# Kernel optimization log

Hardware: AMD Instinct MI355X
Metric: run time of the kernel (lower is better)

The kernel has to match this reference:

```python
import jax, jax.numpy as jnp
import numpy as np

N = 50000
E = 1_600_000
SIGMA = 0.5


def _spmm(rows, cols, vals, dense):
    # sparse [N,N] @ dense [N,D] via gather + segment_sum
    return jax.ops.segment_sum(vals[:, None] * dense[cols], rows, num_segments=N)


def _gnn_layer(h, rows, cols, vals, W, active=True):
    support = h @ W            # [N, out]
    out = _spmm(rows, cols, vals, support)
    return jax.nn.relu(out) if active else out


def setup_inputs() -> dict:
    key = jax.random.key(0)
    ks = jax.random.split(key, 14)
    dims = [512, 500, 500, 2000, 10, 10]  # n_input, enc1, enc2, enc3, n_z, n_clusters
    inp = {
        "x": jax.random.normal(ks[0], (N, dims[0]), dtype=jnp.float32),
        "adj_rows": jax.random.randint(ks[1], (E,), 0, N, dtype=jnp.int32),
        "adj_cols": jax.random.randint(ks[2], (E,), 0, N, dtype=jnp.int32),
        "adj_vals": jax.random.uniform(ks[3], (E,), dtype=jnp.float32),
        "tra1": jax.random.normal(ks[4], (N, dims[1]), dtype=jnp.float32),
        "tra2": jax.random.normal(ks[5], (N, dims[2]), dtype=jnp.float32),
        "tra3": jax.random.normal(ks[6], (N, dims[3]), dtype=jnp.float32),
        "z": jax.random.normal(ks[7], (N, dims[4]), dtype=jnp.float32),
    }
    for i in range(5):
        fan_in, fan_out = dims[i], dims[i + 1]
        bound = float(np.sqrt(6.0 / (fan_in + fan_out)))  # xavier uniform
        inp[f"W{i+1}"] = jax.random.uniform(
            ks[8 + i], (fan_in, fan_out), dtype=jnp.float32, minval=-bound, maxval=bound)
    return inp


def reference(x, adj_rows, adj_cols, adj_vals, tra1, tra2, tra3, z,
              W1, W2, W3, W4, W5):
    s = SIGMA
    h = _gnn_layer(x, adj_rows, adj_cols, adj_vals, W1)
    h = _gnn_layer((1 - s) * h + s * tra1, adj_rows, adj_cols, adj_vals, W2)
    h = _gnn_layer((1 - s) * h + s * tra2, adj_rows, adj_cols, adj_vals, W3)
    h = _gnn_layer((1 - s) * h + s * tra3, adj_rows, adj_cols, adj_vals, W4)
    h = _gnn_layer((1 - s) * h + s * z, adj_rows, adj_cols, adj_vals, W5, active=False)
    return h
```

## Files before the change

kernel.cpp:

```cpp
#include <hip/hip_runtime.h>
#include <hip/hip_bf16.h>


#define SCAN_CHUNK 512
#define BM 128
#define BN 128
#define BK 64

typedef __attribute__((ext_vector_type(4))) float f32x4;
typedef __attribute__((ext_vector_type(8))) __bf16 bf16x8;
typedef __attribute__((ext_vector_type(8))) short s16x8;

__device__ __forceinline__ bf16x8 as_bf(s16x8 v) { union { s16x8 s; bf16x8 b; } u; u.s = v; return u.b; }
__device__ __forceinline__ ushort f2bf(float f) {
    uint u = __float_as_uint(f);
    return (ushort)((u + 0x7FFFu + ((u >> 16) & 1u)) >> 16);
}
__device__ __forceinline__ float bf2f(ushort s) { return __uint_as_float(((uint)s) << 16); }

#define GLL16(g, l)                                                                 \
    __builtin_amdgcn_global_load_lds((const __attribute__((address_space(1))) void*)(g), \
                                     (__attribute__((address_space(3))) void*)(l), 16, 0, 0)

#define STAGE_TILE8(k0, base)                                                       \
    _Pragma("unroll")                                                               \
    for (int i = 0; i < 2; ++i) {                                                   \
        int ar = row0 + arow_off + i * 64;                                          \
        if (ar >= M) ar = M - 1;                                                    \
        GLL16(A + (size_t)ar * 512 + (k0) + acol, &lds[(base) + (w * 8 + i * 64) * BK]); \
        GLL16(Bt + (size_t)(col0 + arow_off + i * 64) * 512 + (k0) + acol,          \
              &lds[(base) + 8192 + (w * 8 + i * 64) * BK]);                         \
    }

#define COMPUTE_TILE8(base)                                                         \
    _Pragma("unroll")                                                               \
    for (int s = 0; s < 2; ++s) {                                                   \
        int cswz = (((s * 4 + (l >> 4)) ^ (l & 7)) << 3);                           \
        bf16x8 af[4], bfr[2];                                                       \
        _Pragma("unroll")                                                           \
        for (int m = 0; m < 4; ++m)                                                 \
            af[m] = as_bf(*(const s16x8*)&lds[(base) + (wr + m * 16 + (l & 15)) * BK + cswz]); \
        _Pragma("unroll")                                                           \
        for (int n = 0; n < 2; ++n)                                                 \
            bfr[n] = as_bf(*(const s16x8*)&lds[(base) + 8192 + (wc + n * 16 + (l & 15)) * BK + cswz]); \
        _Pragma("unroll")                                                           \
        for (int m = 0; m < 4; ++m)                                                 \
            _Pragma("unroll")                                                       \
            for (int n = 0; n < 2; ++n)                                             \
                acc[m][n] = __builtin_amdgcn_mfma_f32_16x16x32_bf16(af[m], bfr[n], acc[m][n], 0, 0, 0); \
    }

#define KLOOP_PIPELINED()                                                           \
    STAGE_TILE8(0, 0);                                                              \
    int base = 0;                                                                   \
    _Pragma("unroll 1")                                                             \
    for (int t = 0; t < 8; ++t) {                                                   \
        if (t < 7) {                                                                \
            STAGE_TILE8((t + 1) * BK, base ^ 16384);                                \
            asm volatile("s_waitcnt vmcnt(4)" ::: "memory");                        \
        } else {                                                                    \
            asm volatile("s_waitcnt vmcnt(0)" ::: "memory");                        \
        }                                                                           \
        __builtin_amdgcn_s_barrier();                                               \
        __builtin_amdgcn_sched_barrier(0);                                          \
        COMPUTE_TILE8(base);                                                        \
        __builtin_amdgcn_sched_barrier(0);                                          \
        __builtin_amdgcn_s_barrier();                                               \
        base ^= 16384;                                                              \
    }

__global__ __launch_bounds__(512) void gemm_sup(const ushort* __restrict__ A,
                                                const ushort* __restrict__ Bt,
                                                ushort* __restrict__ C, int M) {
    __shared__ ushort lds[32768];
    int tid = threadIdx.x;
    int w = tid >> 6, l = tid & 63;
    int row0 = blockIdx.y * BM, col0 = blockIdx.x * BN;
    int wr = (w >> 2) * 64, wc = (w & 3) * 32;
    f32x4 acc[4][2] = {};
    int arow_off = w * 8 + (l >> 3);
    int acol = (((l & 7) ^ (l >> 3)) << 3);

    KLOOP_PIPELINED();

    int crow = (l >> 4) * 4, ccol = l & 15;
#pragma unroll
    for (int m = 0; m < 4; ++m)
#pragma unroll
        for (int n = 0; n < 2; ++n) {
            int gc = col0 + wc + n * 16 + ccol;
#pragma unroll
            for (int r = 0; r < 4; ++r) {
                int gr = row0 + wr + m * 16 + crow + r;
                if (gr < M) C[(size_t)gr * 512 + gc] = f2bf(acc[m][n][r]);
            }
        }
}

__global__ __launch_bounds__(512) void gemm3_w4(const ushort* __restrict__ A,
                                                const ushort* __restrict__ Bt,
                                                const float* __restrict__ T,
                                                const float* __restrict__ W4,
                                                float* __restrict__ sup4p, int M) {
    __shared__ ushort lds[32768];
    int tid = threadIdx.x;
    int w = tid >> 6, l = tid & 63;
    int row0 = blockIdx.y * BM, col0 = blockIdx.x * BN;
    int wr = (w >> 2) * 64, wc = (w & 3) * 32;
    int crow = (l >> 4) * 4, ccol = l & 15;

    bf16x8 w4f;
    {
        s16x8 tmp;
#pragma unroll
        for (int kk = 0; kk < 8; ++kk) {
            int gk = col0 + (w & 3) * 32 + ((l >> 4) << 3) + kk;
            float v = (ccol < 10 && gk < 2000) ? 0.5f * W4[(size_t)gk * 10 + ccol] : 0.f;
            tmp[kk] = (short)f2bf(v);
        }
        w4f = as_bf(tmp);
    }

    f32x4 acc[4][2] = {};
    int arow_off = w * 8 + (l >> 3);
    int acol = (((l & 7) ^ (l >> 3)) << 3);

    KLOOP_PIPELINED();

    ushort* actS = lds;

    __syncthreads();
#pragma unroll
    for (int m = 0; m < 4; ++m)
#pragma unroll
        for (int n = 0; n < 2; ++n) {
            int cl = wc + n * 16 + ccol;
            int cch = cl >> 3, clo = cl & 7;
#pragma unroll
            for (int r = 0; r < 4; ++r) {
                int rl = wr + m * 16 + crow + r;
                actS[rl * 128 + (((cch ^ (rl & 7)) << 3) | clo)] = f2bf(fmaxf(acc[m][n][r], 0.f));
            }
        }
    __syncthreads();

    f32x4 acc2[4] = {};
    {
        int chunk = (w & 3) * 4 + (l >> 4);
#pragma unroll
        for (int m = 0; m < 4; ++m) {
            int row = wr + m * 16 + ccol;
            bf16x8 af = as_bf(*(const s16x8*)&actS[row * 128 + ((chunk ^ (row & 7)) << 3)]);
            acc2[m] = __builtin_amdgcn_mfma_f32_16x16x32_bf16(af, w4f, acc2[m], 0, 0, 0);
        }
    }
    __syncthreads();

    {
        int r_off = tid >> 5;
        int c4 = (tid & 31) * 4;
        int chunk = (tid & 31) >> 1;
        int lo = (tid & 1) * 4;
#pragma unroll
        for (int p = 0; p < 8; ++p) {
            int rl = p * 16 + r_off;
            int gr = row0 + rl;
            int gcb = col0 + c4;
            ushort4 h;
            if (gr < M && gcb + 3 < 2000) {
                float4 tv = *(const float4*)(T + (size_t)gr * 2000 + gcb);
                h.x = f2bf(tv.x); h.y = f2bf(tv.y); h.z = f2bf(tv.z); h.w = f2bf(tv.w);
            } else {
                float e[4];
#pragma unroll
                for (int i = 0; i < 4; ++i)
                    e[i] = (gr < M && gcb + i < 2000) ? T[(size_t)gr * 2000 + gcb + i] : 0.f;
                h.x = f2bf(e[0]); h.y = f2bf(e[1]); h.z = f2bf(e[2]); h.w = f2bf(e[3]);
            }
            *(ushort4*)&actS[rl * 128 + ((chunk ^ (rl & 7)) << 3) + lo] = h;
        }
    }
    __syncthreads();

    {
        int chunk = (w & 3) * 4 + (l >> 4);
#pragma unroll
        for (int m = 0; m < 4; ++m) {
            int row = wr + m * 16 + ccol;
            bf16x8 af = as_bf(*(const s16x8*)&actS[row * 128 + ((chunk ^ (row & 7)) << 3)]);
            acc2[m] = __builtin_amdgcn_mfma_f32_16x16x32_bf16(af, w4f, acc2[m], 0, 0, 0);
        }
    }
    __syncthreads();

    float* redS = (float*)lds;
    {
        int q = w & 3;
#pragma unroll
        for (int m = 0; m < 4; ++m)
#pragma unroll
            for (int r = 0; r < 4; ++r) {
                int row = wr + m * 16 + crow + r;
                redS[(q * 128 + row) * 16 + ccol] = acc2[m][r];
            }
    }
    __syncthreads();
    {
        float* dst = sup4p + (size_t)blockIdx.x * ((size_t)M * 10);
#pragma unroll
        for (int p = 0; p < 4; ++p) {
            int o = p * 512 + tid;
            int row = o >> 4, col = o & 15;
            int gr = row0 + row;
            if (col < 10 && gr < M) {
                float s = redS[(0 * 128 + row) * 16 + col] + redS[(1 * 128 + row) * 16 + col]
                        + redS[(2 * 128 + row) * 16 + col] + redS[(3 * 128 + row) * 16 + col];
                dst[(size_t)gr * 10 + col] = s;
            }
        }
    }
}

__global__ __launch_bounds__(256) void sup4_reduce(const float* __restrict__ P,
                                                   float* __restrict__ O, int n) {
    int i = blockIdx.x * 256 + threadIdx.x;
    if (i >= n) return;
    float s = 0.f;
#pragma unroll
    for (int j = 0; j < 16; ++j) s += P[(size_t)j * n + i];
    O[i] = s;
}

__global__ __launch_bounds__(256) void cvt4(const float* __restrict__ s,
                                            ushort* __restrict__ d, long n4) {
    long i = (long)blockIdx.x * 256 + threadIdx.x;
    if (i >= n4) return;
    float4 v = ((const float4*)s)[i];
    ushort4 o = { f2bf(v.x), f2bf(v.y), f2bf(v.z), f2bf(v.w) };
    ((ushort4*)d)[i] = o;
}

__global__ __launch_bounds__(256) void cvt_wt(const float* __restrict__ W,
                                              ushort* __restrict__ Wt,
                                              int Ksrc, int Nsrc, int Npad) {
    int i = blockIdx.x * 256 + threadIdx.x;
    if (i >= Npad * 512) return;
    int n = i >> 9, k = i & 511;
    float v = (k < Ksrc && n < Nsrc) ? W[(size_t)k * Nsrc + n] : 0.f;
    Wt[i] = f2bf(v);
}

__global__ __launch_bounds__(256) void csr_count(const int* __restrict__ rows,
                                                 int* __restrict__ cnt, int E) {
    int e = blockIdx.x * 256 + threadIdx.x;
    if (e < E) atomicAdd(&cnt[rows[e]], 1);
}

__global__ __launch_bounds__(256) void scan1(const int* __restrict__ cnt,
                                             int* __restrict__ csum, int n) {
    __shared__ int red[256];
    int base = blockIdx.x * SCAN_CHUNK;
    int t = threadIdx.x;
    int s = 0;
    if (base + t < n) s += cnt[base + t];
    if (base + t + 256 < n) s += cnt[base + t + 256];
    red[t] = s;
    __syncthreads();
    for (int off = 128; off; off >>= 1) {
        if (t < off) red[t] += red[t + off];
        __syncthreads();
    }
    if (t == 0) csum[blockIdx.x] = red[0];
}

__global__ void scan2(int* csum, int nch) {
    if (threadIdx.x == 0 && blockIdx.x == 0) {
        int acc = 0;
        for (int i = 0; i < nch; ++i) { int v = csum[i]; csum[i] = acc; acc += v; }
    }
}

__global__ __launch_bounds__(256) void scan3(const int* __restrict__ cnt,
                                             const int* __restrict__ csum,
                                             int* __restrict__ rowptr, int n, int E) {
    __shared__ int sm[SCAN_CHUNK];
    int base = blockIdx.x * SCAN_CHUNK;
    int t = threadIdx.x;
    for (int i = t; i < SCAN_CHUNK; i += 256) sm[i] = (base + i < n) ? cnt[base + i] : 0;
    __syncthreads();
    for (int off = 1; off < SCAN_CHUNK; off <<= 1) {
        int i0 = t, i1 = t + 256;
        int v0 = (i0 >= off) ? sm[i0 - off] : 0;
        int v1 = (i1 >= off) ? sm[i1 - off] : 0;
        __syncthreads();
        sm[i0] += v0;
        sm[i1] += v1;
        __syncthreads();
    }
    int off0 = csum[blockIdx.x];
    for (int i = t; i < SCAN_CHUNK; i += 256)
        if (base + i < n) rowptr[base + i] = off0 + (i ? sm[i - 1] : 0);
    if (blockIdx.x == 0 && t == 0) rowptr[n] = E;
}

__global__ __launch_bounds__(256) void csr_fill(const int* __restrict__ rows,
                                                const int* __restrict__ cols,
                                                const float* __restrict__ vals,
                                                int* __restrict__ cur,
                                                int2* __restrict__ edges, int E) {
    int e = blockIdx.x * 256 + threadIdx.x;
    if (e >= E) return;
    int p = atomicAdd(&cur[rows[e]], 1);
    edges[p] = make_int2(cols[e], __float_as_int(vals[e]));
}

__global__ __launch_bounds__(256) void spmm_bf(const int* __restrict__ rowptr,
                                               const int2* __restrict__ edges,
                                               const ushort* __restrict__ S,
                                               const float* __restrict__ T,
                                               ushort* __restrict__ O,
                                               int nrows, int domix) {
    int wid = (int)((blockIdx.x * 256 + threadIdx.x) >> 6);
    int lane = threadIdx.x & 63;
    if (wid >= nrows) return;
    int beg = rowptr[wid], end = rowptr[wid + 1];
    float acc[8] = {0.f, 0.f, 0.f, 0.f, 0.f, 0.f, 0.f, 0.f};
    int e = beg;
    for (; e + 3 < end; e += 4) {
        int2 e0 = edges[e], e1 = edges[e + 1], e2 = edges[e + 2], e3 = edges[e + 3];
        float v0 = __int_as_float(e0.y), v1 = __int_as_float(e1.y);
        float v2 = __int_as_float(e2.y), v3 = __int_as_float(e3.y);
        s16x8 a = ((const s16x8*)(S + (size_t)e0.x * 512))[lane];
        s16x8 b = ((const s16x8*)(S + (size_t)e1.x * 512))[lane];
        s16x8 c = ((const s16x8*)(S + (size_t)e2.x * 512))[lane];
        s16x8 d = ((const s16x8*)(S + (size_t)e3.x * 512))[lane];
#pragma unroll
        for (int j = 0; j < 8; ++j)
            acc[j] += v0 * bf2f((ushort)a[j]) + v1 * bf2f((ushort)b[j])
                    + v2 * bf2f((ushort)c[j]) + v3 * bf2f((ushort)d[j]);
    }
    for (; e + 1 < end; e += 2) {
        int2 e0 = edges[e], e1 = edges[e + 1];
        float v0 = __int_as_float(e0.y), v1 = __int_as_float(e1.y);
        s16x8 a = ((const s16x8*)(S + (size_t)e0.x * 512))[lane];
        s16x8 b = ((const s16x8*)(S + (size_t)e1.x * 512))[lane];
#pragma unroll
        for (int j = 0; j < 8; ++j)
            acc[j] += v0 * bf2f((ushort)a[j]) + v1 * bf2f((ushort)b[j]);
    }
    if (e < end) {
        int2 e0 = edges[e];
        float v0 = __int_as_float(e0.y);
        s16x8 a = ((const s16x8*)(S + (size_t)e0.x * 512))[lane];
#pragma unroll
        for (int j = 0; j < 8; ++j)
            acc[j] += v0 * bf2f((ushort)a[j]);
    }
    int c0 = lane * 8;
    float res[8];
    if (domix) {
        float tv[8] = {0.f, 0.f, 0.f, 0.f, 0.f, 0.f, 0.f, 0.f};
        const float* trow = T + (size_t)wid * 500;
        if (c0 + 8 <= 500) {
            float4 t0 = *(const float4*)(trow + c0);
            float4 t1 = *(const float4*)(trow + c0 + 4);
            tv[0] = t0.x; tv[1] = t0.y; tv[2] = t0.z; tv[3] = t0.w;
            tv[4] = t1.x; tv[5] = t1.y; tv[6] = t1.z; tv[7] = t1.w;
        } else {
#pragma unroll
            for (int j = 0; j < 8; ++j)
                if (c0 + j < 500) tv[j] = trow[c0 + j];
        }
#pragma unroll
        for (int j = 0; j < 8; ++j)
            res[j] = (c0 + j < 500) ? (0.5f * fmaxf(acc[j], 0.f) + 0.5f * tv[j]) : 0.f;
    } else {
#pragma unroll
        for (int j = 0; j < 8; ++j)
            res[j] = (c0 + j < 500) ? acc[j] : 0.f;
    }
    s16x8 o;
#pragma unroll
    for (int j = 0; j < 8; ++j) o[j] = (short)f2bf(res[j]);
    ((s16x8*)(O + (size_t)wid * 512))[lane] = o;
}

__global__ __launch_bounds__(256) void spmm10(const int* __restrict__ rowptr,
                                              const int2* __restrict__ edges,
                                              const float* __restrict__ S,
                                              const float* __restrict__ T,
                                              const float* __restrict__ W5,
                                              float* __restrict__ O, int nrows) {
    int g = (int)((blockIdx.x * 256 + threadIdx.x) >> 4);
    int t = threadIdx.x & 15;
    if (g >= nrows || t >= 10) return;
    int beg = rowptr[g], end = rowptr[g + 1];
    float acc = 0.f;
    for (int e = beg; e < end; ++e) {
        int2 ed = edges[e];
        acc += __int_as_float(ed.y) * S[(size_t)ed.x * 10 + t];
    }
    if (W5) {
        float m = 0.5f * fmaxf(acc, 0.f) + 0.5f * T[(size_t)g * 10 + t];
        float s5 = 0.f;
#pragma unroll
        for (int i = 0; i < 10; ++i)
            s5 += __shfl(m, i, 16) * W5[i * 10 + t];
        O[(size_t)g * 10 + t] = s5;
    } else {
        O[(size_t)g * 10 + t] = acc;
    }
}

extern "C" void kernel_launch(void* const* d_in, const int* in_sizes, int n_in,
                              void* d_out, int out_size, void* d_ws, size_t ws_size,
                              hipStream_t stream) {
    const float* x    = (const float*)d_in[0];
    const int*   ar   = (const int*)d_in[1];
    const int*   ac   = (const int*)d_in[2];
    const float* av   = (const float*)d_in[3];
    const float* tra1 = (const float*)d_in[4];
    const float* tra2 = (const float*)d_in[5];
    const float* tra3 = (const float*)d_in[6];
    const float* z    = (const float*)d_in[7];
    const float* W1   = (const float*)d_in[8];
    const float* W2   = (const float*)d_in[9];
    const float* W3   = (const float*)d_in[10];
    const float* W4   = (const float*)d_in[11];
    const float* W5   = (const float*)d_in[12];

    const int E = in_sizes[1];
    const int N = in_sizes[7] / 10;
    const int NCH = (N + SCAN_CHUNK - 1) / SCAN_CHUNK;

    ushort* Abf    = (ushort*)d_ws;
    ushort* Sbf    = Abf + (size_t)N * 512;
    ushort* Wt1    = Sbf + (size_t)N * 512;
    ushort* Wt2    = Wt1 + 512 * 512;
    ushort* Wt3    = Wt2 + 512 * 512;
    float*  sup4   = (float*)(Wt3 + 2048 * 512);
    float*  sup5   = sup4 + (size_t)N * 10;
    float*  sup4p  = sup5 + (size_t)N * 10;
    int2*   edges  = (int2*)(sup4p + (size_t)16 * N * 10);
    int*    rowptr = (int*)(edges + E);
    int*    cnt    = rowptr + (N + 1);
    int*    csum   = cnt + N;
    float*  out    = (float*)d_out;

    dim3 blk(256);
    dim3 blk8(512);

    cvt4<<<(int)(((long)N * 512 / 4 + 255) / 256), blk, 0, stream>>>(x, Abf, (long)N * 512 / 4);
    cvt_wt<<<(512 * 512 + 255) / 256, blk, 0, stream>>>(W1, Wt1, 512, 500, 512);
    cvt_wt<<<(512 * 512 + 255) / 256, blk, 0, stream>>>(W2, Wt2, 500, 500, 512);
    cvt_wt<<<(2048 * 512 + 255) / 256, blk, 0, stream>>>(W3, Wt3, 500, 2000, 2048);

    hipMemsetAsync(cnt, 0, (size_t)N * sizeof(int), stream);
    csr_count<<<(E + 255) / 256, blk, 0, stream>>>(ar, cnt, E);
    scan1<<<NCH, blk, 0, stream>>>(cnt, csum, N);
    scan2<<<1, 64, 0, stream>>>(csum, NCH);
    scan3<<<NCH, blk, 0, stream>>>(cnt, csum, rowptr, N, E);
    hipMemcpyAsync(cnt, rowptr, (size_t)N * sizeof(int), hipMemcpyDeviceToDevice, stream);
    csr_fill<<<(E + 255) / 256, blk, 0, stream>>>(ar, ac, av, cnt, edges, E);

    const int spmm_blocks   = (N * 64 + 255) / 256;
    const int spmm10_blocks = (N * 16 + 255) / 256;

    {
        dim3 g(4, (N + BM - 1) / BM);
        gemm_sup<<<g, blk8, 0, stream>>>(Abf, Wt1, Sbf, N);
    }
    spmm_bf<<<spmm_blocks, blk, 0, stream>>>(rowptr, edges, Sbf, tra1, Abf, N, 1);

    {
        dim3 g(4, (N + BM - 1) / BM);
        gemm_sup<<<g, blk8, 0, stream>>>(Abf, Wt2, Sbf, N);
    }
    spmm_bf<<<spmm_blocks, blk, 0, stream>>>(rowptr, edges, Sbf, tra2, Abf, N, 1);

    spmm_bf<<<spmm_blocks, blk, 0, stream>>>(rowptr, edges, Abf, nullptr, Sbf, N, 0);
    {
        dim3 g(16, (N + BM - 1) / BM);
        gemm3_w4<<<g, blk8, 0, stream>>>(Sbf, Wt3, tra3, W4, sup4p, N);
    }
    sup4_reduce<<<(N * 10 + 255) / 256, blk, 0, stream>>>(sup4p, sup4, N * 10);

    spmm10<<<spmm10_blocks, blk, 0, stream>>>(rowptr, edges, sup4, z, W5, sup5, N);

    spmm10<<<spmm10_blocks, blk, 0, stream>>>(rowptr, edges, sup5, nullptr, nullptr, out, N);
}
```

Measured before the change: 1.349 ms.

## Split bf16 SpMM into column slices with edge-parallel lanes and shuffle reduction

The SpMM kernel now splits the 512 feature columns into 8 slices of 64 across grid.y. Within a wavefront, 8 lane groups each take a different subset of edges and the partial sums are combined with xor shuffles. The aim is more parallelism and more memory requests in flight per row, since each lane group processes fewer edges. In exchange, each edge index is reloaded once per slice, row gathers shrink to 128-byte chunks, and the shuffle reduction and mix/store run on only one group of 8 lanes.

```diff
diff --git a/kernel.cpp b/kernel.cpp
--- a/kernel.cpp
+++ b/kernel.cpp
@@ -6,6 +6,7 @@
 #define BM 128
 #define BN 128
 #define BK 64
+#define NSLICE 8
 
 typedef __attribute__((ext_vector_type(4))) float f32x4;
 typedef __attribute__((ext_vector_type(8))) __bf16 bf16x8;
@@ -314,36 +315,26 @@
     edges[p] = make_int2(cols[e], __float_as_int(vals[e]));
 }
 
-__global__ __launch_bounds__(256) void spmm_bf(const int* __restrict__ rowptr,
-                                               const int2* __restrict__ edges,
-                                               const ushort* __restrict__ S,
-                                               const float* __restrict__ T,
-                                               ushort* __restrict__ O,
-                                               int nrows, int domix) {
+__global__ __launch_bounds__(256) void spmm_bfs(const int* __restrict__ rowptr,
+                                                const int2* __restrict__ edges,
+                                                const ushort* __restrict__ S,
+                                                const float* __restrict__ T,
+                                                ushort* __restrict__ O,
+                                                int nrows, int domix) {
     int wid = (int)((blockIdx.x * 256 + threadIdx.x) >> 6);
+    if (wid >= nrows) return;
     int lane = threadIdx.x & 63;
-    if (wid >= nrows) return;
+    int g = lane >> 3, t = lane & 7;
+    int c0 = blockIdx.y * 64 + t * 8;
     int beg = rowptr[wid], end = rowptr[wid + 1];
+
     float acc[8] = {0.f, 0.f, 0.f, 0.f, 0.f, 0.f, 0.f, 0.f};
-    int e = beg;
-    for (; e + 3 < end; e += 4) {
-        int2 e0 = edges[e], e1 = edges[e + 1], e2 = edges[e + 2], e3 = edges[e + 3];
+    int e = beg + g;
+    for (; e + 8 < end; e += 16) {
+        int2 e0 = edges[e], e1 = edges[e + 8];
         float v0 = __int_as_float(e0.y), v1 = __int_as_float(e1.y);
-        float v2 = __int_as_float(e2.y), v3 = __int_as_float(e3.y);
-        s16x8 a = ((const s16x8*)(S + (size_t)e0.x * 512))[lane];
-        s16x8 b = ((const s16x8*)(S + (size_t)e1.x * 512))[lane];
-        s16x8 c = ((const s16x8*)(S + (size_t)e2.x * 512))[lane];
-        s16x8 d = ((const s16x8*)(S + (size_t)e3.x * 512))[lane];
-#pragma unroll
-        for (int j = 0; j < 8; ++j)
-            acc[j] += v0 * bf2f((ushort)a[j]) + v1 * bf2f((ushort)b[j])
-                    + v2 * bf2f((ushort)c[j]) + v3 * bf2f((ushort)d[j]);
-    }
-    for (; e + 1 < end; e += 2) {
-        int2 e0 = edges[e], e1 = edges[e + 1];
-        float v0 = __int_as_float(e0.y), v1 = __int_as_float(e1.y);
-        s16x8 a = ((const s16x8*)(S + (size_t)e0.x * 512))[lane];
-        s16x8 b = ((const s16x8*)(S + (size_t)e1.x * 512))[lane];
+        s16x8 a = *(const s16x8*)(S + (size_t)e0.x * 512 + c0);
+        s16x8 b = *(const s16x8*)(S + (size_t)e1.x * 512 + c0);
 #pragma unroll
         for (int j = 0; j < 8; ++j)
             acc[j] += v0 * bf2f((ushort)a[j]) + v1 * bf2f((ushort)b[j]);
@@ -351,12 +342,19 @@
     if (e < end) {
         int2 e0 = edges[e];
         float v0 = __int_as_float(e0.y);
-        s16x8 a = ((const s16x8*)(S + (size_t)e0.x * 512))[lane];
+        s16x8 a = *(const s16x8*)(S + (size_t)e0.x * 512 + c0);
 #pragma unroll
         for (int j = 0; j < 8; ++j)
             acc[j] += v0 * bf2f((ushort)a[j]);
     }
-    int c0 = lane * 8;
+
+#pragma unroll
+    for (int off = 8; off <= 32; off <<= 1)
+#pragma unroll
+        for (int j = 0; j < 8; ++j)
+            acc[j] += __shfl_xor(acc[j], off, 64);
+
+    if (g != 0) return;
     float res[8];
     if (domix) {
         float tv[8] = {0.f, 0.f, 0.f, 0.f, 0.f, 0.f, 0.f, 0.f};
@@ -382,7 +380,7 @@
     s16x8 o;
 #pragma unroll
     for (int j = 0; j < 8; ++j) o[j] = (short)f2bf(res[j]);
-    ((s16x8*)(O + (size_t)wid * 512))[lane] = o;
+    *(s16x8*)(O + (size_t)wid * 512 + c0) = o;
 }
 
 __global__ __launch_bounds__(256) void spmm10(const int* __restrict__ rowptr,
@@ -463,22 +461,22 @@
     hipMemcpyAsync(cnt, rowptr, (size_t)N * sizeof(int), hipMemcpyDeviceToDevice, stream);
     csr_fill<<<(E + 255) / 256, blk, 0, stream>>>(ar, ac, av, cnt, edges, E);
 
-    const int spmm_blocks   = (N * 64 + 255) / 256;
+    dim3 spmm_grid((N * 64 + 255) / 256, NSLICE);
     const int spmm10_blocks = (N * 16 + 255) / 256;
 
     {
         dim3 g(4, (N + BM - 1) / BM);
         gemm_sup<<<g, blk8, 0, stream>>>(Abf, Wt1, Sbf, N);
     }
-    spmm_bf<<<spmm_blocks, blk, 0, stream>>>(rowptr, edges, Sbf, tra1, Abf, N, 1);
+    spmm_bfs<<<spmm_grid, blk, 0, stream>>>(rowptr, edges, Sbf, tra1, Abf, N, 1);
 
     {
         dim3 g(4, (N + BM - 1) / BM);
         gemm_sup<<<g, blk8, 0, stream>>>(Abf, Wt2, Sbf, N);
     }
-    spmm_bf<<<spmm_blocks, blk, 0, stream>>>(rowptr, edges, Sbf, tra2, Abf, N, 1);
-
-    spmm_bf<<<spmm_blocks, blk, 0, stream>>>(rowptr, edges, Abf, nullptr, Sbf, N, 0);
+    spmm_bfs<<<spmm_grid, blk, 0, stream>>>(rowptr, edges, Sbf, tra2, Abf, N, 1);
+
+    spmm_bfs<<<spmm_grid, blk, 0, stream>>>(rowptr, edges, Abf, nullptr, Sbf, N, 0);
     {
         dim3 g(16, (N + BM - 1) / BM);
         gemm3_w4<<<g, blk8, 0, stream>>>(Sbf, Wt3, tra3, W4, sup4p, N);
```

Measured after the change: 1.363 ms. About the same (+1.0%).
